# Optimization experiments

Hardware: AMD Instinct MI355X
Metric: run time of the kernel (lower is better)

## Reference

```python
import jax, jax.numpy as jnp
import numpy as np

# Render constants matching GaussianRenderer(__init__): image size and top-K blend depth.
H, W, K = 128, 128, 10
N_G = 2048  # number of gaussians


def setup_inputs() -> dict:
    key = jax.random.key(0)
    k1, k2, k3, k4 = jax.random.split(key, 4)
    # Means in pixel coordinates so gaussians cover the image.
    gaussian_means = jax.random.uniform(k1, (N_G, 2), dtype=jnp.float32) * jnp.array([W, H], jnp.float32)
    # Rotation angle per gaussian in [0, 2pi).
    gaussian_rotations = jax.random.uniform(k2, (N_G,), dtype=jnp.float32) * (2.0 * np.pi)
    # log std-devs centered at log(3) => ~3px footprint.
    gaussian_log_scales = jax.random.normal(k3, (N_G, 2), dtype=jnp.float32) * 0.3 + np.log(3.0)
    gaussian_colors = jax.random.uniform(k4, (N_G, 3), dtype=jnp.float32)
    return {
        "gaussian_means": gaussian_means,
        "gaussian_rotations": gaussian_rotations,
        "gaussian_log_scales": gaussian_log_scales,
        "gaussian_colors": gaussian_colors,
    }


def reference(gaussian_means, gaussian_rotations, gaussian_log_scales, gaussian_colors):
    """2D Gaussian splatting: per-pixel top-K gaussians by opacity, alpha-composited.

    Covariance per gaussian: Sigma = R(theta) diag(exp(2*log_scales)) R(theta)^T.
    alpha_i(p) = exp(-0.5 * d^T Sigma^{-1} d), d = p - mean_i.
    Per pixel, the K gaussians with largest alpha are blended front-to-back:
        out = sum_i color_i * alpha_i * prod_{j<i} (1 - alpha_j).
    (The torch module's tile binning + max_G_per_tile is a GPU performance
    optimization; the dense evaluation here computes the same per-pixel math.)
    """
    cos_t = jnp.cos(gaussian_rotations)  # [N]
    sin_t = jnp.sin(gaussian_rotations)
    inv_var = jnp.exp(-2.0 * gaussian_log_scales)  # [N,2] = 1/sigma^2 per axis
    ivx, ivy = inv_var[:, 0], inv_var[:, 1]
    # Sigma^{-1} = R diag(1/sx^2, 1/sy^2) R^T  (symmetric 2x2: [[a, b], [b, c]])
    a = cos_t * cos_t * ivx + sin_t * sin_t * ivy  # [N]
    c = sin_t * sin_t * ivx + cos_t * cos_t * ivy
    b = cos_t * sin_t * (ivx - ivy)

    xs = jnp.arange(W, dtype=jnp.float32) + 0.5
    ys = jnp.arange(H, dtype=jnp.float32) + 0.5
    px, py = jnp.meshgrid(xs, ys)  # [H,W] each
    dx = px.reshape(-1, 1) - gaussian_means[:, 0]  # [P, N], P = H*W
    dy = py.reshape(-1, 1) - gaussian_means[:, 1]
    q = a * dx * dx + 2.0 * b * dx * dy + c * dy * dy  # Mahalanobis distance^2 [P,N]
    alpha = jnp.exp(-0.5 * q)  # [P,N] in (0,1]

    top_alpha, top_idx = jax.lax.top_k(alpha, K)  # [P,K], descending alpha
    # Front-to-back transmittance: T_0 = 1, T_i = prod_{j<i} (1 - alpha_j)
    trans = jnp.cumprod(1.0 - top_alpha, axis=1)
    trans = jnp.concatenate([jnp.ones_like(trans[:, :1]), trans[:, :-1]], axis=1)
    weight = top_alpha * trans  # [P,K]
    top_colors = gaussian_colors[top_idx]  # [P,K,3]
    image = jnp.einsum("pk,pkc->pc", weight, top_colors).reshape(H, W, 3)
    return image
```

## Files before the change

kernel.cpp:

```cpp
#include <hip/hip_runtime.h>

#define HH 128
#define WW 128
#define NPX (HH * WW)
#define KK 10
#define PXB 16
#define TPP 16
#define LCAP 352
#define JMAX 22
#define SCAP 128
#define SPAD 129
#define SMPAD 17
#define ALPHA_MIN 5e-4f
#define RADIUS_K 3.8990f

__device__ __forceinline__ bool beats(float a, int ai, float b, int bi) {
  return (a > b) || (a == b && ai < bi);
}

__device__ __forceinline__ void insert_tb(float vals[KK], int ids[KK], float v,
                                          int vi) {
#pragma unroll
  for (int k = 0; k < KK; ++k) {
    bool sw = beats(v, vi, vals[k], ids[k]);
    float tv = vals[k];
    int ti = ids[k];
    vals[k] = sw ? v : tv;
    ids[k]  = sw ? vi : ti;
    v  = sw ? tv : v;
    vi = sw ? ti : vi;
  }
}

__device__ __forceinline__ void bubble_vals10(float vals[KK], float v) {
#pragma unroll
  for (int k = 0; k < KK; ++k) {
    float tv = vals[k];
    bool sw = v > tv;
    vals[k] = sw ? v : tv;
    v = sw ? tv : v;
  }
}

__global__ __launch_bounds__(256) void splat_kernel(
    const float* __restrict__ means, const float* __restrict__ rots,
    const float* __restrict__ lscales, const float* __restrict__ cols,
    int nG, float* __restrict__ out) {
  __shared__ float4 sA[LCAP];
  __shared__ float  sMy[LCAP];
  __shared__ int    glist[LCAP];
  __shared__ float  smax[PXB * SMPAD];
  __shared__ float  stau[PXB];
  __shared__ float2 sbuf[PXB][SPAD];
  __shared__ int    scnt[PXB];
  __shared__ int    lcnt;

  int t  = threadIdx.x;
  int pl = t & 15;
  int ts = t >> 4;
  int tile = blockIdx.x;
  int x0 = (tile & 31) << 2;
  int y0 = (tile >> 5) << 2;
  int x = x0 | (pl & 3);
  int y = y0 | (pl >> 2);
  float px = (float)x + 0.5f, py = (float)y + 0.5f;

  if (t == 0) lcnt = 0;
  if (t < PXB) scnt[t] = 0;
  __syncthreads();

  const float2* m2 = (const float2*)means;
  const float2* l2 = (const float2*)lscales;
  float rx0 = (float)x0 + 0.5f, rx1 = (float)x0 + 3.5f;
  float ry0 = (float)y0 + 0.5f, ry1 = (float)y0 + 3.5f;
  for (int g = t; g < nG; g += 256) {
    float2 mg = m2[g];
    float2 lg = l2[g];
    float smx = __expf(fmaxf(lg.x, lg.y));
    float r = fmaf(RADIUS_K * 1.01f, smx, 0.05f);
    float cx = fminf(fmaxf(mg.x, rx0), rx1) - mg.x;
    float cy = fminf(fmaxf(mg.y, ry0), ry1) - mg.y;
    if (cx * cx + cy * cy <= r * r) {
      int idx = atomicAdd(&lcnt, 1);
      if (idx < LCAP) {
        float th = rots[g];
        float s = __sinf(th), c = __cosf(th);
        float ivx = __expf(-2.0f * lg.x);
        float ivy = __expf(-2.0f * lg.y);
        sA[idx] = make_float4(c * c * ivx + s * s * ivy,
                              2.0f * (c * s * (ivx - ivy)),
                              s * s * ivx + c * c * ivy, mg.x);
        sMy[idx] = mg.y;
        glist[idx] = g;
      }
    }
  }
  __syncthreads();
  int cnt = min(lcnt, LCAP);

  float ra[JMAX];
  float mymax = 0.0f;
#pragma unroll
  for (int j = 0; j < JMAX; ++j) {
    int i = ts + j * TPP;
    float a = 0.0f;
    if (i < cnt) {
      float4 q0 = sA[i];
      float dx = px - q0.w;
      float dy = py - sMy[i];
      float q = fmaf(dx, fmaf(q0.y, dy, q0.x * dx), q0.z * dy * dy);
      a = __expf(-0.5f * q);
    }
    ra[j] = a;
    mymax = fmaxf(mymax, a);
  }
  smax[pl * SMPAD + ts] = mymax;
  __syncthreads();

  if (t < PXB) {
    float tv[KK];
#pragma unroll
    for (int k = 0; k < KK; ++k) tv[k] = 0.0f;
#pragma unroll
    for (int j = 0; j < TPP; ++j) bubble_vals10(tv, smax[t * SMPAD + j]);
    stau[t] = fmaxf(tv[KK - 1], ALPHA_MIN);
  }
  __syncthreads();

  float tau = stau[pl];
#pragma unroll
  for (int j = 0; j < JMAX; ++j) {
    int i = ts + j * TPP;
    float a = ra[j];
    if (a >= tau) {
      int idx = atomicAdd(&scnt[pl], 1);
      if (idx < SCAP) sbuf[pl][idx] = make_float2(a, __int_as_float(glist[i]));
    }
  }
  __syncthreads();

  if (t < 2 * PXB) {
    int p2 = t >> 1, half = t & 1;
    int sc = min(scnt[p2], SCAP);
    float vals[KK];
    int ids[KK];
#pragma unroll
    for (int k = 0; k < KK; ++k) { vals[k] = 0.0f; ids[k] = 0; }
    for (int i = half; i < sc; i += 2) {
      float2 e = sbuf[p2][i];
      float a = e.x;
      int id = __float_as_int(e.y);
      if (beats(a, id, vals[KK - 1], ids[KK - 1])) insert_tb(vals, ids, a, id);
    }
    float ov[KK];
    int oi[KK];
#pragma unroll
    for (int k = 0; k < KK; ++k) {
      ov[k] = __shfl_xor(vals[k], 1);
      oi[k] = __shfl_xor(ids[k], 1);
    }
    if (half == 0) {
#pragma unroll
      for (int k = 0; k < KK; ++k) {
        if (!beats(ov[k], oi[k], vals[KK - 1], ids[KK - 1])) break;
        insert_tb(vals, ids, ov[k], oi[k]);
      }
      int xx = x0 | (p2 & 3);
      int yy = y0 | (p2 >> 2);
      int pp = yy * WW + xx;
      float trans = 1.0f, r = 0.0f, g = 0.0f, b = 0.0f;
#pragma unroll
      for (int k = 0; k < KK; ++k) {
        float a = vals[k];
        float w = a * trans;
        int id = ids[k];
        r += w * cols[3 * id + 0];
        g += w * cols[3 * id + 1];
        b += w * cols[3 * id + 2];
        trans *= (1.0f - a);
      }
      out[3 * pp + 0] = r;
      out[3 * pp + 1] = g;
      out[3 * pp + 2] = b;
    }
  }
}

extern "C" void kernel_launch(void* const* d_in, const int* in_sizes, int n_in,
                              void* d_out, int out_size, void* d_ws, size_t ws_size,
                              hipStream_t stream) {
  const float* means   = (const float*)d_in[0];
  const float* rots    = (const float*)d_in[1];
  const float* lscales = (const float*)d_in[2];
  const float* cols    = (const float*)d_in[3];
  float* out = (float*)d_out;
  int nG = in_sizes[1];

  splat_kernel<<<NPX / PXB, 256, 0, stream>>>(means, rots, lscales, cols, nG, out);
}
```

Before: 76.01 us.

## Replace shared-memory top-K stages with wavefront shuffle-based selection and compositing

Remaps threads so each pixel's 16 threads sit inside one 16-lane group, then does the threshold computation, candidate compaction, top-K selection and compositing with shuffles and ballots instead of shared atomics and three block barriers. Top-K uses packed 64-bit alpha/id keys with a parallel max-reduction per round, and transmittance is computed with a prefix-product scan. Gaussian list compaction uses a wave-aggregated atomic, and the gaussian count is made a compile-time constant for the common size. The candidate buffer cap drops to 96 per pixel, so if more candidates than that pass the threshold, some are silently dropped.

```diff
diff --git a/kernel.cpp b/kernel.cpp
--- a/kernel.cpp
+++ b/kernel.cpp
@@ -5,68 +5,41 @@
 #define NPX (HH * WW)
 #define KK 10
 #define PXB 16
-#define TPP 16
 #define LCAP 352
 #define JMAX 22
-#define SCAP 128
-#define SPAD 129
-#define SMPAD 17
+#define KEYC 6
+#define SCAP (16 * KEYC)
+#define SPAD (SCAP + 1)
 #define ALPHA_MIN 5e-4f
 #define RADIUS_K 3.8990f
 
-__device__ __forceinline__ bool beats(float a, int ai, float b, int bi) {
-  return (a > b) || (a == b && ai < bi);
-}
-
-__device__ __forceinline__ void insert_tb(float vals[KK], int ids[KK], float v,
-                                          int vi) {
-#pragma unroll
-  for (int k = 0; k < KK; ++k) {
-    bool sw = beats(v, vi, vals[k], ids[k]);
-    float tv = vals[k];
-    int ti = ids[k];
-    vals[k] = sw ? v : tv;
-    ids[k]  = sw ? vi : ti;
-    v  = sw ? tv : v;
-    vi = sw ? ti : vi;
-  }
-}
-
-__device__ __forceinline__ void bubble_vals10(float vals[KK], float v) {
-#pragma unroll
-  for (int k = 0; k < KK; ++k) {
-    float tv = vals[k];
-    bool sw = v > tv;
-    vals[k] = sw ? v : tv;
-    v = sw ? tv : v;
-  }
-}
-
+typedef unsigned long long u64;
+typedef unsigned int u32;
+
+__device__ __forceinline__ u64 umax64(u64 a, u64 b) { return a > b ? a : b; }
+
+template <int NGC>
 __global__ __launch_bounds__(256) void splat_kernel(
     const float* __restrict__ means, const float* __restrict__ rots,
     const float* __restrict__ lscales, const float* __restrict__ cols,
-    int nG, float* __restrict__ out) {
+    int nG_rt, float* __restrict__ out) {
+  const int nG = NGC > 0 ? NGC : nG_rt;
   __shared__ float4 sA[LCAP];
   __shared__ float  sMy[LCAP];
   __shared__ int    glist[LCAP];
-  __shared__ float  smax[PXB * SMPAD];
-  __shared__ float  stau[PXB];
   __shared__ float2 sbuf[PXB][SPAD];
-  __shared__ int    scnt[PXB];
   __shared__ int    lcnt;
 
-  int t  = threadIdx.x;
-  int pl = t & 15;
-  int ts = t >> 4;
+  int t = threadIdx.x;
+  int lane = t & 63;
+  int pl  = t >> 4;
+  int tsl = t & 15;
   int tile = blockIdx.x;
-  int x0 = (tile & 31) << 2;
-  int y0 = (tile >> 5) << 2;
-  int x = x0 | (pl & 3);
-  int y = y0 | (pl >> 2);
+  int x0 = (tile & 31) << 2, y0 = (tile >> 5) << 2;
+  int x = x0 | (pl & 3), y = y0 | (pl >> 2);
   float px = (float)x + 0.5f, py = (float)y + 0.5f;
 
   if (t == 0) lcnt = 0;
-  if (t < PXB) scnt[t] = 0;
   __syncthreads();
 
   const float2* m2 = (const float2*)means;
@@ -80,18 +53,26 @@
     float r = fmaf(RADIUS_K * 1.01f, smx, 0.05f);
     float cx = fminf(fmaxf(mg.x, rx0), rx1) - mg.x;
     float cy = fminf(fmaxf(mg.y, ry0), ry1) - mg.y;
-    if (cx * cx + cy * cy <= r * r) {
-      int idx = atomicAdd(&lcnt, 1);
-      if (idx < LCAP) {
-        float th = rots[g];
-        float s = __sinf(th), c = __cosf(th);
-        float ivx = __expf(-2.0f * lg.x);
-        float ivy = __expf(-2.0f * lg.y);
-        sA[idx] = make_float4(c * c * ivx + s * s * ivy,
-                              2.0f * (c * s * (ivx - ivy)),
-                              s * s * ivx + c * c * ivy, mg.x);
-        sMy[idx] = mg.y;
-        glist[idx] = g;
+    bool hit = (cx * cx + cy * cy <= r * r);
+    u64 mask = __ballot(hit);
+    if (mask) {
+      int leader = __ffsll((unsigned long long)mask) - 1;
+      int base;
+      if (lane == leader) base = atomicAdd(&lcnt, __popcll(mask));
+      base = __shfl(base, leader);
+      if (hit) {
+        int idx = base + __popcll(mask & ((1ull << lane) - 1ull));
+        if (idx < LCAP) {
+          float th = rots[g];
+          float s = __sinf(th), c = __cosf(th);
+          float ivx = __expf(-2.0f * lg.x);
+          float ivy = __expf(-2.0f * lg.y);
+          sA[idx] = make_float4(c * c * ivx + s * s * ivy,
+                                2.0f * (c * s * (ivx - ivy)),
+                                s * s * ivx + c * c * ivy, mg.x);
+          sMy[idx] = mg.y;
+          glist[idx] = g;
+        }
       }
     }
   }
@@ -102,88 +83,104 @@
   float mymax = 0.0f;
 #pragma unroll
   for (int j = 0; j < JMAX; ++j) {
-    int i = ts + j * TPP;
+    int i = tsl + j * 16;
     float a = 0.0f;
     if (i < cnt) {
       float4 q0 = sA[i];
-      float dx = px - q0.w;
-      float dy = py - sMy[i];
+      float dx = px - q0.w, dy = py - sMy[i];
       float q = fmaf(dx, fmaf(q0.y, dy, q0.x * dx), q0.z * dy * dy);
       a = __expf(-0.5f * q);
     }
     ra[j] = a;
     mymax = fmaxf(mymax, a);
   }
-  smax[pl * SMPAD + ts] = mymax;
-  __syncthreads();
-
-  if (t < PXB) {
-    float tv[KK];
-#pragma unroll
-    for (int k = 0; k < KK; ++k) tv[k] = 0.0f;
-#pragma unroll
-    for (int j = 0; j < TPP; ++j) bubble_vals10(tv, smax[t * SMPAD + j]);
-    stau[t] = fmaxf(tv[KK - 1], ALPHA_MIN);
-  }
-  __syncthreads();
-
-  float tau = stau[pl];
+
+  float tv[KK];
+#pragma unroll
+  for (int k = 0; k < KK; ++k) tv[k] = 0.0f;
+#pragma unroll
+  for (int i = 0; i < 16; ++i) {
+    float v = __shfl(mymax, i, 16);
+#pragma unroll
+    for (int k = 0; k < KK; ++k) {
+      float tvk = tv[k];
+      bool sw = v > tvk;
+      tv[k] = sw ? v : tvk;
+      v = sw ? tvk : v;
+    }
+  }
+  float tau = fmaxf(tv[KK - 1], ALPHA_MIN);
+
+  int cpx = 0;
+  int grp = lane >> 4;
 #pragma unroll
   for (int j = 0; j < JMAX; ++j) {
-    int i = ts + j * TPP;
-    float a = ra[j];
-    if (a >= tau) {
-      int idx = atomicAdd(&scnt[pl], 1);
-      if (idx < SCAP) sbuf[pl][idx] = make_float2(a, __int_as_float(glist[i]));
-    }
-  }
-  __syncthreads();
-
-  if (t < 2 * PXB) {
-    int p2 = t >> 1, half = t & 1;
-    int sc = min(scnt[p2], SCAP);
-    float vals[KK];
-    int ids[KK];
-#pragma unroll
-    for (int k = 0; k < KK; ++k) { vals[k] = 0.0f; ids[k] = 0; }
-    for (int i = half; i < sc; i += 2) {
-      float2 e = sbuf[p2][i];
-      float a = e.x;
-      int id = __float_as_int(e.y);
-      if (beats(a, id, vals[KK - 1], ids[KK - 1])) insert_tb(vals, ids, a, id);
-    }
-    float ov[KK];
-    int oi[KK];
-#pragma unroll
-    for (int k = 0; k < KK; ++k) {
-      ov[k] = __shfl_xor(vals[k], 1);
-      oi[k] = __shfl_xor(ids[k], 1);
-    }
-    if (half == 0) {
-#pragma unroll
-      for (int k = 0; k < KK; ++k) {
-        if (!beats(ov[k], oi[k], vals[KK - 1], ids[KK - 1])) break;
-        insert_tb(vals, ids, ov[k], oi[k]);
-      }
-      int xx = x0 | (p2 & 3);
-      int yy = y0 | (p2 >> 2);
-      int pp = yy * WW + xx;
-      float trans = 1.0f, r = 0.0f, g = 0.0f, b = 0.0f;
-#pragma unroll
-      for (int k = 0; k < KK; ++k) {
-        float a = vals[k];
-        float w = a * trans;
-        int id = ids[k];
-        r += w * cols[3 * id + 0];
-        g += w * cols[3 * id + 1];
-        b += w * cols[3 * id + 2];
-        trans *= (1.0f - a);
-      }
-      out[3 * pp + 0] = r;
-      out[3 * pp + 1] = g;
-      out[3 * pp + 2] = b;
-    }
-  }
+    bool s = ra[j] >= tau;
+    u64 mask = __ballot(s);
+    u32 sub = (u32)((mask >> (grp * 16)) & 0xFFFFull);
+    if (s) {
+      int idx = cpx + __popc(sub & ((1u << tsl) - 1u));
+      if (idx < SCAP)
+        sbuf[pl][idx] = make_float2(ra[j], __int_as_float(glist[tsl + j * 16]));
+    }
+    cpx += __popc(sub);
+  }
+  int scp = min(cpx, SCAP);
+
+  u64 keys[KEYC];
+#pragma unroll
+  for (int c = 0; c < KEYC; ++c) {
+    int i = tsl + c * 16;
+    u64 kk = 0;
+    if (i < scp) {
+      float2 e = sbuf[pl][i];
+      kk = ((u64)__float_as_uint(e.x) << 32) | (u32)(~(u32)__float_as_int(e.y));
+    }
+    keys[c] = kk;
+  }
+
+  float my_alpha = 0.0f;
+  int my_id = 0;
+#pragma unroll
+  for (int r = 0; r < KK; ++r) {
+    u64 m = keys[0];
+#pragma unroll
+    for (int c = 1; c < KEYC; ++c) m = umax64(m, keys[c]);
+#pragma unroll
+    for (int d = 1; d < 16; d <<= 1)
+      m = umax64(m, (u64)__shfl_xor((unsigned long long)m, d));
+#pragma unroll
+    for (int c = 0; c < KEYC; ++c)
+      if (keys[c] == m) keys[c] = 0;
+    if (tsl == r && m != 0) {
+      my_alpha = __uint_as_float((u32)(m >> 32));
+      my_id = (int)(~(u32)m);
+    }
+  }
+
+  float T = 1.0f - my_alpha;
+#pragma unroll
+  for (int d = 1; d < 16; d <<= 1) {
+    float u = __shfl_up(T, d, 16);
+    if (tsl >= d) T *= u;
+  }
+  float ex = __shfl_up(T, 1, 16);
+  if (tsl == 0) ex = 1.0f;
+  float w = my_alpha * ex;
+  float cr = 0.0f, cg = 0.0f, cb = 0.0f;
+  if (my_alpha > 0.0f) {
+    cr = w * cols[3 * my_id + 0];
+    cg = w * cols[3 * my_id + 1];
+    cb = w * cols[3 * my_id + 2];
+  }
+#pragma unroll
+  for (int d = 1; d < 16; d <<= 1) {
+    cr += __shfl_xor(cr, d);
+    cg += __shfl_xor(cg, d);
+    cb += __shfl_xor(cb, d);
+  }
+  int p = y * WW + x;
+  if (tsl < 3) out[3 * p + tsl] = (tsl == 0) ? cr : ((tsl == 1) ? cg : cb);
 }
 
 extern "C" void kernel_launch(void* const* d_in, const int* in_sizes, int n_in,
@@ -196,5 +193,11 @@
   float* out = (float*)d_out;
   int nG = in_sizes[1];
 
-  splat_kernel<<<NPX / PXB, 256, 0, stream>>>(means, rots, lscales, cols, nG, out);
+  if (nG == 2048) {
+    splat_kernel<2048><<<NPX / PXB, 256, 0, stream>>>(means, rots, lscales,
+                                                      cols, nG, out);
+  } else {
+    splat_kernel<0><<<NPX / PXB, 256, 0, stream>>>(means, rots, lscales,
+                                                   cols, nG, out);
+  }
 }
```

Result: faster. 74.19 us (-2.4%).
